# Performance work log

Hardware: AMD Instinct MI355X
Metric: run time of the kernel (lower is better)

## Reference

```python
import jax, jax.numpy as jnp
import numpy as np

B, S, D, V = 32, 1024, 768, 32000


def setup_inputs() -> dict:
    key = jax.random.key(0)
    ks = jax.random.split(key, 12)
    scale = 0.02
    return {
        "tokens": jax.random.randint(ks[0], (B, S), 0, V, dtype=jnp.int32),
        "mask": jax.random.randint(ks[1], (B, S), 0, 2, dtype=jnp.int32),
        "emb": jax.random.normal(ks[2], (V, D), dtype=jnp.float32) * scale,
        "wq": jax.random.normal(ks[3], (D, D), dtype=jnp.float32) * scale,
        "wk": jax.random.normal(ks[4], (D, D), dtype=jnp.float32) * scale,
        "wv": jax.random.normal(ks[5], (D, D), dtype=jnp.float32) * scale,
        "ln_g": jnp.ones((D,), dtype=jnp.float32),
        "ln_b": jnp.zeros((D,), dtype=jnp.float32),
        "w1": jax.random.normal(ks[6], (D, D), dtype=jnp.float32) * scale,
        "b1": jnp.zeros((D,), dtype=jnp.float32),
        "wh": jax.random.normal(ks[7], (D, 2), dtype=jnp.float32) * scale,
        "bh": jnp.zeros((2,), dtype=jnp.float32),
    }


def reference(tokens, mask, emb, wq, wk, wv, ln_g, ln_b, w1, b1, wh, bh):
    # embedding lookup: [B,S,D]
    x = emb[tokens]
    q = x @ wq
    k = x @ wk
    v = x @ wv
    # unscaled attention scores: [B,S,S]
    s = jnp.einsum("bsd,btd->bst", q, k)
    # additive padding mask (mask==1 -> -1e9), broadcast over query dim
    s = s + (-1e9) * mask.astype(s.dtype)[:, None, :]
    a = jax.nn.softmax(s, axis=-1)
    o = jnp.einsum("bst,btd->bsd", a, v)
    # classify on first token
    cls = o[:, 0, :]  # [B,D]
    mu = jnp.mean(cls, axis=-1, keepdims=True)
    var = jnp.var(cls, axis=-1, keepdims=True)
    h = (cls - mu) * jax.lax.rsqrt(var + 1e-5) * ln_g + ln_b
    h = jax.nn.gelu(h @ w1 + b1, approximate=False)
    logits = h @ wh + bh  # [B,2]
    return (logits, a)
```

## Files before the change

### kernel.cpp

```cpp
#include <hip/hip_runtime.h>
#include <hip/hip_bf16.h>

#define NB 32
#define SS 1024
#define DD 768

typedef __attribute__((ext_vector_type(8))) short bf16x8;
typedef __attribute__((ext_vector_type(4))) float f32x4;

__device__ inline ushort f2bf(float f) {
    union { float f; unsigned u; } x;
    x.f = f;
    unsigned r = (x.u + 0x7fffu + ((x.u >> 16) & 1u)) >> 16;
    return (ushort)r;
}

#define GLOBAL_PTR(x) ((const __attribute__((address_space(1))) void*)(x))
#define LDS_PTR(x)    ((__attribute__((address_space(3))) void*)(x))

__global__ void k_cvt(const float* __restrict__ wq, const float* __restrict__ wk,
                      ushort* __restrict__ wqb, ushort* __restrict__ wkb) {
    const int i = (blockIdx.x * 256 + threadIdx.x) * 4;
    const float* src = blockIdx.y ? wk : wq;
    ushort* dst = blockIdx.y ? wkb : wqb;
    const float4 v = *(const float4*)(src + i);
    ushort4 o;
    o.x = f2bf(v.x); o.y = f2bf(v.y); o.z = f2bf(v.z); o.w = f2bf(v.w);
    *(ushort4*)(dst + i) = o;
}

__global__ void k_gather(const int* __restrict__ tokens, const float* __restrict__ emb,
                         ushort* __restrict__ xb) {
    int i = (blockIdx.x * 256 + threadIdx.x) * 4;
    int row = i / DD;
    int col = i - row * DD;
    int tok = tokens[row];
    const float4 v = *(const float4*)(emb + (size_t)tok * DD + col);
    ushort4 o;
    o.x = f2bf(v.x); o.y = f2bf(v.y); o.z = f2bf(v.z); o.w = f2bf(v.w);
    *(ushort4*)(xb + (size_t)row * DD + col) = o;
}

template <int MODE>
__global__ __launch_bounds__(256, 2) void k_gemm(const ushort* __restrict__ A,
                                                 const ushort* __restrict__ Bt,
                                                 ushort* __restrict__ Cb,
                                                 float* __restrict__ Cs) {
    constexpr int BK = 64;
    __shared__ ushort As[128 * BK];
    __shared__ ushort Bs[128 * BK];
    const int tid = threadIdx.x;
    const int wave = tid >> 6, lane = tid & 63;
    const int ld = DD;
    size_t abase = (size_t)blockIdx.x * 128 * ld;
    size_t bbase = (size_t)blockIdx.y * 128 * ld;
    if (MODE == 1) {
        size_t z = blockIdx.z;
        abase += z * (size_t)SS * DD;
        bbase += z * (size_t)SS * DD;
    }
    f32x4 acc[4][4] = {};
    const int r = tid >> 3;
    const int cc = (tid & 7) * 8;
    const int wm = (wave >> 1) * 64, wn = (wave & 1) * 64;
    const int lr = lane & 15, lc = (lane >> 4) * 8;

    for (int k0 = 0; k0 < DD; k0 += BK) {
        __syncthreads();
#pragma unroll
        for (int i = 0; i < 4; i++) {
            __builtin_amdgcn_global_load_lds(GLOBAL_PTR(A + abase + (size_t)(r + i * 32) * ld + k0 + cc),
                                             LDS_PTR(As + (r + i * 32) * BK + cc), 16, 0, 0);
            __builtin_amdgcn_global_load_lds(GLOBAL_PTR(Bt + bbase + (size_t)(r + i * 32) * ld + k0 + cc),
                                             LDS_PTR(Bs + (r + i * 32) * BK + cc), 16, 0, 0);
        }
        __syncthreads();
#pragma unroll
        for (int kk = 0; kk < 2; kk++) {
            bf16x8 af[4], bfv[4];
#pragma unroll
            for (int m = 0; m < 4; m++)
                af[m] = *(const bf16x8*)(As + (wm + m * 16 + lr) * BK + kk * 32 + lc);
#pragma unroll
            for (int n = 0; n < 4; n++)
                bfv[n] = *(const bf16x8*)(Bs + (wn + n * 16 + lr) * BK + kk * 32 + lc);
#pragma unroll
            for (int m = 0; m < 4; m++)
#pragma unroll
                for (int n = 0; n < 4; n++)
                    acc[m][n] = __builtin_amdgcn_mfma_f32_16x16x32_bf16(af[m], bfv[n], acc[m][n], 0, 0, 0);
        }
    }

    const int rowbase = blockIdx.x * 128 + wm + (lane >> 4) * 4;
    if (MODE == 0) {
        const int colbase = blockIdx.y * 128 + wn + (lane & 15);
#pragma unroll
        for (int m = 0; m < 4; m++)
#pragma unroll
            for (int n = 0; n < 4; n++)
#pragma unroll
                for (int j = 0; j < 4; j++)
                    Cb[(size_t)(rowbase + m * 16 + j) * DD + colbase + n * 16] = f2bf(acc[m][n][j]);
    } else {
        float* Co = Cs + (size_t)blockIdx.z * SS * SS;
        const int colbase = blockIdx.y * 128 + wn + (lane & 15);
#pragma unroll
        for (int m = 0; m < 4; m++)
#pragma unroll
            for (int n = 0; n < 4; n++)
#pragma unroll
                for (int j = 0; j < 4; j++)
                    Co[(size_t)(rowbase + m * 16 + j) * SS + colbase + n * 16] = acc[m][n][j];
    }
}

__global__ __launch_bounds__(256) void k_softmax(float* __restrict__ a, const int* __restrict__ mask) {
    const int rid = blockIdx.x;
    const int b = rid >> 10, rr = rid & 1023;
    float* row = a + (size_t)b * SS * SS + (size_t)rr * SS;
    const int* mrow = mask + b * SS;
    const int t = threadIdx.x * 4;
    float4 v = *(float4*)(row + t);
    const int4 mk = *(const int4*)(mrow + t);
    float x0 = v.x + (mk.x ? -1e9f : 0.0f);
    float x1 = v.y + (mk.y ? -1e9f : 0.0f);
    float x2 = v.z + (mk.z ? -1e9f : 0.0f);
    float x3 = v.w + (mk.w ? -1e9f : 0.0f);
    float mx = fmaxf(fmaxf(x0, x1), fmaxf(x2, x3));
#pragma unroll
    for (int off = 32; off; off >>= 1) mx = fmaxf(mx, __shfl_xor(mx, off));
    __shared__ float redm[4], reds[4];
    if ((threadIdx.x & 63) == 0) redm[threadIdx.x >> 6] = mx;
    __syncthreads();
    mx = fmaxf(fmaxf(redm[0], redm[1]), fmaxf(redm[2], redm[3]));
    float e0 = expf(x0 - mx), e1 = expf(x1 - mx), e2 = expf(x2 - mx), e3 = expf(x3 - mx);
    float sm = e0 + e1 + e2 + e3;
#pragma unroll
    for (int off = 32; off; off >>= 1) sm += __shfl_xor(sm, off);
    if ((threadIdx.x & 63) == 0) reds[threadIdx.x >> 6] = sm;
    __syncthreads();
    sm = reds[0] + reds[1] + reds[2] + reds[3];
    const float inv = 1.0f / sm;
    v.x = e0 * inv; v.y = e1 * inv; v.z = e2 * inv; v.w = e3 * inv;
    *(float4*)(row + t) = v;
}

__global__ __launch_bounds__(256) void k_xbar(const float* __restrict__ a, const int* __restrict__ tokens,
                                              const float* __restrict__ emb, float* __restrict__ part) {
    const int b = blockIdx.x >> 3, c = blockIdx.x & 7;
    __shared__ float a0s[128];
    __shared__ int toks[128];
    const int tid = threadIdx.x;
    if (tid < 128) {
        a0s[tid] = a[(size_t)b * SS * SS + c * 128 + tid];
        toks[tid] = tokens[b * SS + c * 128 + tid];
    }
    __syncthreads();
    float acc0 = 0.f, acc1 = 0.f, acc2 = 0.f;
#pragma unroll 4
    for (int t = 0; t < 128; t++) {
        const float at = a0s[t];
        const float* er = emb + (size_t)toks[t] * DD;
        acc0 = fmaf(at, er[tid], acc0);
        acc1 = fmaf(at, er[tid + 256], acc1);
        acc2 = fmaf(at, er[tid + 512], acc2);
    }
    float* p = part + ((size_t)c * NB + b) * DD;
    p[tid] = acc0; p[tid + 256] = acc1; p[tid + 512] = acc2;
}

__global__ __launch_bounds__(128) void k_cls(const float* __restrict__ part, const float* __restrict__ wv,
                                             float* __restrict__ cls) {
    const int b = blockIdx.y, tid = threadIdx.x;
    const int c = blockIdx.x * 128 + tid;
    __shared__ float xb[DD];
#pragma unroll
    for (int j = 0; j < 6; j++) {
        const int k = tid + j * 128;
        float s = 0.f;
#pragma unroll
        for (int p = 0; p < 8; p++) s += part[((size_t)p * NB + b) * DD + k];
        xb[k] = s;
    }
    __syncthreads();
    float acc = 0.f;
#pragma unroll 8
    for (int k = 0; k < DD; k++) acc = fmaf(xb[k], wv[(size_t)k * DD + c], acc);
    cls[(size_t)b * DD + c] = acc;
}

__device__ inline float block_sum256(float v, float* red, int tid) {
#pragma unroll
    for (int off = 32; off; off >>= 1) v += __shfl_xor(v, off);
    __syncthreads();
    if ((tid & 63) == 0) red[tid >> 6] = v;
    __syncthreads();
    return red[0] + red[1] + red[2] + red[3];
}

__global__ __launch_bounds__(256) void k_ln(const float* __restrict__ cls, const float* __restrict__ ln_g,
                                            const float* __restrict__ ln_b, float* __restrict__ hs) {
    const int b = blockIdx.x, tid = threadIdx.x;
    __shared__ float red[4];
    float v[3];
#pragma unroll
    for (int j = 0; j < 3; j++) v[j] = cls[(size_t)b * DD + tid + j * 256];
    const float mu = block_sum256(v[0] + v[1] + v[2], red, tid) * (1.0f / DD);
    float dv = 0.f;
#pragma unroll
    for (int j = 0; j < 3; j++) { const float d = v[j] - mu; dv += d * d; }
    __syncthreads();
    const float var = block_sum256(dv, red, tid) * (1.0f / DD);
    const float sc = 1.0f / sqrtf(var + 1e-5f);
#pragma unroll
    for (int j = 0; j < 3; j++) {
        const int d = tid + j * 256;
        hs[(size_t)b * DD + d] = (v[j] - mu) * sc * ln_g[d] + ln_b[d];
    }
}

__global__ __launch_bounds__(128) void k_mlp(const float* __restrict__ hs, const float* __restrict__ w1,
                                             const float* __restrict__ b1, const float* __restrict__ wh,
                                             float* __restrict__ part_l) {
    const int b = blockIdx.y, tid = threadIdx.x;
    const int j = blockIdx.x * 128 + tid;
    __shared__ float h[DD];
#pragma unroll
    for (int q = 0; q < 6; q++) h[tid + q * 128] = hs[(size_t)b * DD + tid + q * 128];
    __syncthreads();
    float p = b1[j];
#pragma unroll 8
    for (int d = 0; d < DD; d++) p = fmaf(h[d], w1[(size_t)d * DD + j], p);
    const float g = 0.5f * p * (1.0f + erff(p * 0.70710678118654752f));
    float l0 = g * wh[j * 2 + 0];
    float l1 = g * wh[j * 2 + 1];
#pragma unroll
    for (int off = 32; off; off >>= 1) { l0 += __shfl_xor(l0, off); l1 += __shfl_xor(l1, off); }
    __shared__ float r0[2], r1[2];
    if ((tid & 63) == 0) { r0[tid >> 6] = l0; r1[tid >> 6] = l1; }
    __syncthreads();
    if (tid == 0) {
        part_l[((size_t)b * 6 + blockIdx.x) * 2 + 0] = r0[0] + r0[1];
        part_l[((size_t)b * 6 + blockIdx.x) * 2 + 1] = r1[0] + r1[1];
    }
}

__global__ __launch_bounds__(64) void k_final(const float* __restrict__ part_l, const float* __restrict__ bh,
                                              float* __restrict__ out) {
    const int b = threadIdx.x;
    if (b < NB) {
        float l0 = bh[0], l1 = bh[1];
#pragma unroll
        for (int c = 0; c < 6; c++) {
            l0 += part_l[((size_t)b * 6 + c) * 2 + 0];
            l1 += part_l[((size_t)b * 6 + c) * 2 + 1];
        }
        out[b * 2 + 0] = l0;
        out[b * 2 + 1] = l1;
    }
}

extern "C" void kernel_launch(void* const* d_in, const int* in_sizes, int n_in,
                              void* d_out, int out_size, void* d_ws, size_t ws_size,
                              hipStream_t stream) {
    const int*   tokens = (const int*)d_in[0];
    const int*   mask   = (const int*)d_in[1];
    const float* emb    = (const float*)d_in[2];
    const float* wq     = (const float*)d_in[3];
    const float* wk     = (const float*)d_in[4];
    const float* wv     = (const float*)d_in[5];
    const float* ln_g   = (const float*)d_in[6];
    const float* ln_b   = (const float*)d_in[7];
    const float* w1     = (const float*)d_in[8];
    const float* b1     = (const float*)d_in[9];
    const float* wh     = (const float*)d_in[10];
    const float* bh     = (const float*)d_in[11];
    float* out = (float*)d_out;

    char* ws = (char*)d_ws;
    const size_t XB = (size_t)NB * SS * DD * 2;
    const size_t WB = (size_t)DD * DD * 2;
    ushort* xb  = (ushort*)ws;
    ushort* yb  = (ushort*)(ws + XB);
    ushort* wqb = (ushort*)(ws + 2 * XB);
    ushort* wkb = (ushort*)(ws + 2 * XB + WB);
    ushort* Wt  = (ushort*)(ws + 2 * XB + 2 * WB);
    char*   p4  = ws + 2 * XB + 3 * WB;
    float*  part   = (float*)p4;
    float*  cls    = (float*)(p4 + 786432);
    float*  hsb    = (float*)(p4 + 786432 + 98304);
    float*  part_l = (float*)(p4 + 786432 + 2 * 98304);

    float* s_region = out + 64;

    k_cvt<<<dim3(576, 2), 256, 0, stream>>>(wq, wk, wqb, wkb);
    k_gather<<<24576, 256, 0, stream>>>(tokens, emb, xb);
    k_gemm<0><<<dim3(6, 6), 256, 0, stream>>>(wkb, wqb, Wt, nullptr);
    k_gemm<0><<<dim3(256, 6), 256, 0, stream>>>(xb, Wt, yb, nullptr);
    k_gemm<1><<<dim3(8, 8, 32), 256, 0, stream>>>(yb, xb, nullptr, s_region);
    k_softmax<<<32768, 256, 0, stream>>>(s_region, mask);
    k_xbar<<<256, 256, 0, stream>>>(s_region, tokens, emb, part);
    k_cls<<<dim3(6, NB), 128, 0, stream>>>(part, wv, cls);
    k_ln<<<NB, 256, 0, stream>>>(cls, ln_g, ln_b, hsb);
    k_mlp<<<dim3(6, NB), 128, 0, stream>>>(hsb, w1, b1, wh, part_l);
    k_final<<<1, 64, 0, stream>>>(part_l, bh, out);
}
```

Baseline: 369.3 us.

## Double-buffer GEMM LDS tiles and remap score-GEMM workgroups across batches

The GEMM kernel now uses two LDS buffers so the async global-to-LDS load of the next K tile is issued before the MFMA work on the current tile. This removes one barrier per iteration and the load stall that came with it. The batched score GEMM also moves to a 1D grid whose workgroup IDs interleave 8 batches. The likely intent is to spread each batch's blocks across XCDs/L2 for better locality. The cost is double the LDS per block (64 KB), which may limit occupancy against the launch bound of 2 blocks per CU.

```diff
diff --git a/kernel.cpp b/kernel.cpp
--- a/kernel.cpp
+++ b/kernel.cpp
@@ -47,54 +47,75 @@
                                                  ushort* __restrict__ Cb,
                                                  float* __restrict__ Cs) {
     constexpr int BK = 64;
-    __shared__ ushort As[128 * BK];
-    __shared__ ushort Bs[128 * BK];
+    __shared__ ushort As[2][128 * BK];
+    __shared__ ushort Bs[2][128 * BK];
     const int tid = threadIdx.x;
     const int wave = tid >> 6, lane = tid & 63;
-    const int ld = DD;
-    size_t abase = (size_t)blockIdx.x * 128 * ld;
-    size_t bbase = (size_t)blockIdx.y * 128 * ld;
+
+    int bx, by;
+    size_t abase, bbase;
     if (MODE == 1) {
-        size_t z = blockIdx.z;
-        abase += z * (size_t)SS * DD;
-        bbase += z * (size_t)SS * DD;
-    }
-    f32x4 acc[4][4] = {};
+        const int wgid = blockIdx.x;
+        const int g = wgid >> 9, w = wgid & 511;
+        const int b = g * 8 + (w & 7);
+        const int tile = w >> 3;
+        bx = tile & 7; by = tile >> 3;
+        abase = (size_t)b * SS * DD + (size_t)bx * 128 * DD;
+        bbase = (size_t)b * SS * DD + (size_t)by * 128 * DD;
+        Cs += (size_t)b * SS * SS;
+    } else {
+        bx = blockIdx.x; by = blockIdx.y;
+        abase = (size_t)bx * 128 * DD;
+        bbase = (size_t)by * 128 * DD;
+    }
+
     const int r = tid >> 3;
     const int cc = (tid & 7) * 8;
+
+    auto stage = [&](int buf, int k0) {
+#pragma unroll
+        for (int i = 0; i < 4; i++) {
+            __builtin_amdgcn_global_load_lds(GLOBAL_PTR(A + abase + (size_t)(r + i * 32) * DD + k0 + cc),
+                                             LDS_PTR(&As[buf][(r + i * 32) * BK + cc]), 16, 0, 0);
+            __builtin_amdgcn_global_load_lds(GLOBAL_PTR(Bt + bbase + (size_t)(r + i * 32) * DD + k0 + cc),
+                                             LDS_PTR(&Bs[buf][(r + i * 32) * BK + cc]), 16, 0, 0);
+        }
+    };
+
+    f32x4 acc[4][4] = {};
     const int wm = (wave >> 1) * 64, wn = (wave & 1) * 64;
     const int lr = lane & 15, lc = (lane >> 4) * 8;
 
+    stage(0, 0);
+    __syncthreads();
+    int cur = 0;
+#pragma unroll 1
     for (int k0 = 0; k0 < DD; k0 += BK) {
-        __syncthreads();
-#pragma unroll
-        for (int i = 0; i < 4; i++) {
-            __builtin_amdgcn_global_load_lds(GLOBAL_PTR(A + abase + (size_t)(r + i * 32) * ld + k0 + cc),
-                                             LDS_PTR(As + (r + i * 32) * BK + cc), 16, 0, 0);
-            __builtin_amdgcn_global_load_lds(GLOBAL_PTR(Bt + bbase + (size_t)(r + i * 32) * ld + k0 + cc),
-                                             LDS_PTR(Bs + (r + i * 32) * BK + cc), 16, 0, 0);
-        }
-        __syncthreads();
+        if (k0 + BK < DD) stage(cur ^ 1, k0 + BK);
+        const ushort* as = As[cur];
+        const ushort* bs = Bs[cur];
 #pragma unroll
         for (int kk = 0; kk < 2; kk++) {
             bf16x8 af[4], bfv[4];
 #pragma unroll
             for (int m = 0; m < 4; m++)
-                af[m] = *(const bf16x8*)(As + (wm + m * 16 + lr) * BK + kk * 32 + lc);
+                af[m] = *(const bf16x8*)(as + (wm + m * 16 + lr) * BK + kk * 32 + lc);
 #pragma unroll
             for (int n = 0; n < 4; n++)
-                bfv[n] = *(const bf16x8*)(Bs + (wn + n * 16 + lr) * BK + kk * 32 + lc);
+                bfv[n] = *(const bf16x8*)(bs + (wn + n * 16 + lr) * BK + kk * 32 + lc);
 #pragma unroll
             for (int m = 0; m < 4; m++)
 #pragma unroll
                 for (int n = 0; n < 4; n++)
                     acc[m][n] = __builtin_amdgcn_mfma_f32_16x16x32_bf16(af[m], bfv[n], acc[m][n], 0, 0, 0);
         }
-    }
-
-    const int rowbase = blockIdx.x * 128 + wm + (lane >> 4) * 4;
+        __syncthreads();
+        cur ^= 1;
+    }
+
+    const int rowbase = bx * 128 + wm + (lane >> 4) * 4;
+    const int colbase = by * 128 + wn + (lane & 15);
     if (MODE == 0) {
-        const int colbase = blockIdx.y * 128 + wn + (lane & 15);
 #pragma unroll
         for (int m = 0; m < 4; m++)
 #pragma unroll
@@ -103,15 +124,13 @@
                 for (int j = 0; j < 4; j++)
                     Cb[(size_t)(rowbase + m * 16 + j) * DD + colbase + n * 16] = f2bf(acc[m][n][j]);
     } else {
-        float* Co = Cs + (size_t)blockIdx.z * SS * SS;
-        const int colbase = blockIdx.y * 128 + wn + (lane & 15);
 #pragma unroll
         for (int m = 0; m < 4; m++)
 #pragma unroll
             for (int n = 0; n < 4; n++)
 #pragma unroll
                 for (int j = 0; j < 4; j++)
-                    Co[(size_t)(rowbase + m * 16 + j) * SS + colbase + n * 16] = acc[m][n][j];
+                    Cs[(size_t)(rowbase + m * 16 + j) * SS + colbase + n * 16] = acc[m][n][j];
     }
 }
 
@@ -298,7 +317,7 @@
     k_gather<<<24576, 256, 0, stream>>>(tokens, emb, xb);
     k_gemm<0><<<dim3(6, 6), 256, 0, stream>>>(wkb, wqb, Wt, nullptr);
     k_gemm<0><<<dim3(256, 6), 256, 0, stream>>>(xb, Wt, yb, nullptr);
-    k_gemm<1><<<dim3(8, 8, 32), 256, 0, stream>>>(yb, xb, nullptr, s_region);
+    k_gemm<1><<<2048, 256, 0, stream>>>(yb, xb, nullptr, s_region);
     k_softmax<<<32768, 256, 0, stream>>>(s_region, mask);
     k_xbar<<<256, 256, 0, stream>>>(s_region, tokens, emb, part);
     k_cls<<<dim3(6, NB), 128, 0, stream>>>(part, wv, cls);
```

After: 379.3 us. 2.7% more time.
